# Optimization experiments

Measured on AMD Instinct MI355X. Metric: run time of the kernel, lower is better.

The kernel has to match this reference:

```python
import jax, jax.numpy as jnp
import numpy as np

D = 1024        # node_dim
L = 4           # n_layers
H = 16          # n_heads
HID = 512       # mlp_hidden
NT = 65536      # N_tiles (256x256 board)
U = 4096        # eligible units
NY = 256        # board width


def setup_inputs() -> dict:
    key = jax.random.key(0)
    ks = jax.random.split(key, 32)
    p = lambda i, shape: jax.random.normal(ks[i], shape, jnp.float32) * 0.02
    inp = {
        "node_emb": jax.random.normal(ks[0], (NT, D), jnp.float32),
        "tile_ids": jax.random.randint(ks[1], (U,), 0, NT),
        "entropies": jax.random.uniform(ks[2], (U,), jnp.float32),
        "Ny": NY,
        # input_proj: Linear(D+1, D), torch weight layout (out, in)
        "in_w": p(3, (D, D + 1)), "in_b": p(4, (D,)),
        # per-layer MHA params stacked over L
        "attn_in_w": p(5, (L, 3 * D, D)), "attn_in_b": p(6, (L, 3 * D)),
        "attn_out_w": p(7, (L, D, D)), "attn_out_b": p(8, (L, D)),
        # per-layer FFN: Linear(D, 2D) -> ReLU -> Linear(2D, D)
        "ff_w1": p(9, (L, 2 * D, D)), "ff_b1": p(10, (L, 2 * D)),
        "ff_w2": p(11, (L, D, 2 * D)), "ff_b2": p(12, (L, D)),
        "ln1_g": jnp.ones((L, D), jnp.float32), "ln1_b": jnp.zeros((L, D), jnp.float32),
        "ln2_g": jnp.ones((L, D), jnp.float32), "ln2_b": jnp.zeros((L, D), jnp.float32),
        # score head: D -> HID -> HID -> 1 (mlp_depth=2)
        "sh_w0": p(13, (HID, D)), "sh_b0": p(14, (HID,)),
        "sh_w1": p(15, (HID, HID)), "sh_b1": p(16, (HID,)),
        "sh_w2": p(17, (1, HID)), "sh_b2": p(18, (1,)),
    }
    return inp


def _rope_1d(x, pos):
    half = x.shape[-1] // 2
    theta = 1.0 / (10000.0 ** (jnp.arange(half, dtype=jnp.float32) / half))
    ang = pos[:, None] * theta[None, :]            # (U, half)
    c, s = jnp.cos(ang), jnp.sin(ang)
    x1, x2 = x[..., :half], x[..., half:]
    return jnp.concatenate([x1 * c - x2 * s, x1 * s + x2 * c], axis=-1)


def _ln(x, g, b, eps=1e-5):
    m = x.mean(-1, keepdims=True)
    v = ((x - m) ** 2).mean(-1, keepdims=True)
    return (x - m) / jnp.sqrt(v + eps) * g + b


def reference(node_emb, tile_ids, entropies, Ny, in_w, in_b,
              attn_in_w, attn_in_b, attn_out_w, attn_out_b,
              ff_w1, ff_b1, ff_w2, ff_b2, ln1_g, ln1_b, ln2_g, ln2_b,
              sh_w0, sh_b0, sh_w1, sh_b1, sh_w2, sh_b2):
    u = node_emb[tile_ids]                                   # (U, D)
    x = jnp.concatenate([u, entropies[:, None]], axis=-1) @ in_w.T + in_b
    n_units, d = x.shape
    half = d // 2
    hd = d // H
    rows = (tile_ids // Ny).astype(jnp.float32)
    cols = (tile_ids % Ny).astype(jnp.float32)
    for l in range(L):
        # 2D RoPE: row rotation on first half of dims, col rotation on second
        xr = jnp.concatenate([_rope_1d(x[:, :half], rows),
                              _rope_1d(x[:, half:], cols)], axis=-1)
        wq, wk, wv = jnp.split(attn_in_w[l], 3, axis=0)
        bq, bk, bv = jnp.split(attn_in_b[l], 3, axis=0)
        q = (xr @ wq.T + bq).reshape(n_units, H, hd)
        k = (xr @ wk.T + bk).reshape(n_units, H, hd)
        v = (x @ wv.T + bv).reshape(n_units, H, hd)          # V from un-roped x
        scores = jnp.einsum("qhd,khd->hqk", q, k) / jnp.sqrt(jnp.float32(hd))
        attn = jax.nn.softmax(scores, axis=-1)
        o = jnp.einsum("hqk,khd->qhd", attn, v).reshape(n_units, d)
        o = o @ attn_out_w[l].T + attn_out_b[l]
        x = _ln(x + o, ln1_g[l], ln1_b[l])
        h = jax.nn.relu(x @ ff_w1[l].T + ff_b1[l]) @ ff_w2[l].T + ff_b2[l]
        x = _ln(x + h, ln2_g[l], ln2_b[l])
    h = jax.nn.relu(x @ sh_w0.T + sh_b0)
    h = jax.nn.relu(h @ sh_w1.T + sh_b1)
    logits = (h @ sh_w2.T + sh_b2).squeeze(-1)               # (U,)
    probs = jax.nn.softmax(logits)
    entropy = -(probs * jnp.log(probs + 1e-12)).sum()
    return (probs, entropy, logits)
```

## Files before the change

kernel.cpp:

```cpp
#include <hip/hip_runtime.h>
#include <hip/hip_bf16.h>
#include <math.h>

#define UN 4096
#define DN 1024
#define LN_ 4
#define HN 16
#define HD 64

typedef __attribute__((ext_vector_type(8))) short bf16x8;
typedef __attribute__((ext_vector_type(4))) float f32x4;

__device__ __forceinline__ short f2bf(float f) {
  union { float f; unsigned u; } x; x.f = f;
  unsigned r = x.u + 0x7fffu + ((x.u >> 16) & 1u);
  return (short)(r >> 16);
}
__device__ __forceinline__ float bf2f(short b) {
  union { unsigned u; float f; } x; x.u = ((unsigned)(unsigned short)b) << 16;
  return x.f;
}

__device__ __forceinline__ void gload16(const void* g, void* l) {
  __builtin_amdgcn_global_load_lds(
      (const __attribute__((address_space(1))) void*)g,
      (__attribute__((address_space(3))) void*)l, 16, 0, 0);
}

__global__ __launch_bounds__(256)
void convw_kernel(const float* __restrict__ src, short* __restrict__ dst)
{
  int i = blockIdx.x * 256 + threadIdx.x;
  float4 f0 = ((const float4*)src)[i * 2];
  float4 f1 = ((const float4*)src)[i * 2 + 1];
  bf16x8 o;
  o[0] = f2bf(f0.x); o[1] = f2bf(f0.y); o[2] = f2bf(f0.z); o[3] = f2bf(f0.w);
  o[4] = f2bf(f1.x); o[5] = f2bf(f1.y); o[6] = f2bf(f1.z); o[7] = f2bf(f1.w);
  ((bf16x8*)dst)[i] = o;
}

__global__ __launch_bounds__(256)
void convw_in_kernel(const float* __restrict__ src, short* __restrict__ dst)
{
  int idx = blockIdx.x * 256 + threadIdx.x;
  int r = idx >> 10, c = idx & 1023;
  dst[idx] = f2bf(src[r * 1025 + c]);
}

template<int TM>
__global__ __launch_bounds__(256)
void gemm_bf16(const short* __restrict__ A, int lda,
               const short* __restrict__ W, int ldw,
               const float* __restrict__ bias,
               float* __restrict__ C32, short* __restrict__ C16, int ldc,
               int K, int relu,
               const float* __restrict__ ent, const float* __restrict__ wcol,
               int wstride)
{
  constexpr int MBF = TM / 32;
  constexpr int AIN = TM / 64;
  __shared__ __align__(16) short As[TM][32];
  __shared__ __align__(16) short Ws[128][32];

  const int tid  = threadIdx.x;
  const int bm = blockIdx.x, bn = blockIdx.y;
  const int lane = tid & 63, wave = tid >> 6;
  const int n = lane & 15, quad = lane >> 4;
  const int mw = (wave >> 1) * (TM / 2), nw = (wave & 1) * 64;

  f32x4 acc[MBF][4];
#pragma unroll
  for (int mb = 0; mb < MBF; mb++)
#pragma unroll
    for (int nb = 0; nb < 4; nb++)
#pragma unroll
      for (int r = 0; r < 4; r++) acc[mb][nb][r] = 0.f;

  const int sr = lane >> 2;
  const int sc = (lane & 3) * 8;
  const short* aSrc[AIN]; short* aDst[AIN];
#pragma unroll
  for (int i = 0; i < AIN; i++) {
    aSrc[i] = A + (size_t)(bm * TM + wave * (16 * AIN) + i * 16 + sr) * lda + sc;
    aDst[i] = &As[wave * (16 * AIN) + i * 16][0];
  }
  const short* wSrc[2]; short* wDst[2];
#pragma unroll
  for (int i = 0; i < 2; i++) {
    wSrc[i] = W + (size_t)(bn * 128 + wave * 32 + i * 16 + sr) * ldw + sc;
    wDst[i] = &Ws[wave * 32 + i * 16][0];
  }

  for (int kk = 0; kk < K; kk += 32) {
    __syncthreads();
#pragma unroll
    for (int i = 0; i < AIN; i++) gload16(aSrc[i] + kk, aDst[i]);
#pragma unroll
    for (int i = 0; i < 2; i++)   gload16(wSrc[i] + kk, wDst[i]);
    __syncthreads();

    bf16x8 af[MBF], bfr[4];
#pragma unroll
    for (int mb = 0; mb < MBF; mb++) af[mb] = *(bf16x8*)&As[mw + mb * 16 + n][quad * 8];
#pragma unroll
    for (int nb = 0; nb < 4; nb++)   bfr[nb] = *(bf16x8*)&Ws[nw + nb * 16 + n][quad * 8];
#pragma unroll
    for (int mb = 0; mb < MBF; mb++)
#pragma unroll
      for (int nb = 0; nb < 4; nb++)
        acc[mb][nb] = __builtin_amdgcn_mfma_f32_16x16x32_bf16(af[mb], bfr[nb], acc[mb][nb], 0, 0, 0);
  }

#pragma unroll
  for (int mb = 0; mb < MBF; mb++) {
    float entv[4];
#pragma unroll
    for (int r = 0; r < 4; r++)
      entv[r] = ent ? ent[bm * TM + mw + mb * 16 + quad * 4 + r] : 0.f;
#pragma unroll
    for (int nb = 0; nb < 4; nb++) {
      const int col = bn * 128 + nw + nb * 16 + n;
      const float bs = bias[col];
      const float wc = ent ? wcol[(size_t)col * wstride] : 0.f;
#pragma unroll
      for (int r = 0; r < 4; r++) {
        const int row = bm * TM + mw + mb * 16 + quad * 4 + r;
        float v = acc[mb][nb][r] + bs;
        if (ent)  v += entv[r] * wc;
        if (relu) v = fmaxf(v, 0.f);
        if (C32) C32[(size_t)row * ldc + col] = v;
        if (C16) C16[(size_t)row * ldc + col] = f2bf(v);
      }
    }
  }
}

__global__ __launch_bounds__(256)
void gather_conv_kernel(const float* __restrict__ emb, const int* __restrict__ ids,
                        short* __restrict__ dst)
{
  int idx = blockIdx.x * 256 + threadIdx.x;
  int u = idx >> 10;
  dst[idx] = f2bf(emb[(size_t)ids[u] * 1024 + (idx & 1023)]);
}

__global__ __launch_bounds__(256)
void rope_kernel(const float* __restrict__ x, short* __restrict__ xr,
                 const int* __restrict__ ids, const int* __restrict__ nyp)
{
  int idx = blockIdx.x * 256 + threadIdx.x;
  int u = idx >> 10, j = idx & 1023;
  int blk = j >> 9, o = j & 511;
  int i = o & 255;
  int t = ids[u];
  int ny = *nyp;
  float pos = (blk == 0) ? (float)(t / ny) : (float)(t % ny);
  float theta = expf((float)i * -0.0359778921f);
  float ang = pos * theta;
  float c = cosf(ang), sn = sinf(ang);
  const float* xrow = x + (size_t)u * 1024 + blk * 512;
  float x1 = xrow[i];
  float x2 = xrow[256 + i];
  xr[idx] = f2bf((o < 256) ? (x1 * c - x2 * sn) : (x1 * sn + x2 * c));
}

__global__ __launch_bounds__(256)
void attn_mfma_kernel(const short* __restrict__ qk, const short* __restrict__ v,
                      short* __restrict__ o)
{
  __shared__ __align__(16) short Kt[64][64];
  __shared__ __align__(16) short Vt[64][64];
  __shared__ __align__(16) short Pb[4][16][64];

  const int tid  = threadIdx.x;
  const int lane = tid & 63;
  const int wave = tid >> 6;
  const int head = blockIdx.y;
  const int qb   = blockIdx.x;

  const int n    = lane & 15;
  const int quad = lane >> 4;

  bf16x8 qfrag[2];
  {
    const int qrow = qb * 64 + wave * 16 + n;
    const short* qptr = qk + (size_t)qrow * 2048 + head * 64 + quad * 8;
#pragma unroll
    for (int c = 0; c < 2; c++)
#pragma unroll
      for (int j = 0; j < 8; j++)
        qfrag[c][j] = f2bf(bf2f(qptr[c * 32 + j]) * 0.125f);
  }

  float m_r[4], l_r[4];
  f32x4 o_acc[4];
#pragma unroll
  for (int r = 0; r < 4; r++) { m_r[r] = -3.0e38f; l_r[r] = 0.f; }
#pragma unroll
  for (int nb = 0; nb < 4; nb++)
#pragma unroll
    for (int r = 0; r < 4; r++) o_acc[nb][r] = 0.f;

  const int skey = tid & 63;
  const int sd0  = wave * 16;
  const int krx  = (skey & 7) << 4;

  char* KtB = (char*)&Kt[0][0];
  char* VtB = (char*)&Vt[0][0];
  char* PbB = (char*)&Pb[wave][0][0];

  for (int kt = 0; kt < 64; kt++) {
    __syncthreads();
    {
      const short* kp = qk + (size_t)(kt * 64 + skey) * 2048 + 1024 + head * 64 + sd0;
      bf16x8 k0 = *(const bf16x8*)(kp);
      bf16x8 k1 = *(const bf16x8*)(kp + 8);
      *(bf16x8*)(KtB + skey * 128 + ((sd0 * 2)      ^ krx)) = k0;
      *(bf16x8*)(KtB + skey * 128 + ((sd0 * 2 + 16) ^ krx)) = k1;
      const short* vp = v + (size_t)(kt * 64 + skey) * 1024 + head * 64 + sd0;
      bf16x8 v0 = *(const bf16x8*)(vp);
      bf16x8 v1 = *(const bf16x8*)(vp + 8);
#pragma unroll
      for (int i = 0; i < 8; i++) {
        int d = sd0 + i;
        *(short*)(VtB + d * 128 + ((2 * skey) ^ ((d & 7) << 4))) = v0[i];
      }
#pragma unroll
      for (int i = 0; i < 8; i++) {
        int d = sd0 + 8 + i;
        *(short*)(VtB + d * 128 + ((2 * skey) ^ ((d & 7) << 4))) = v1[i];
      }
    }
    __syncthreads();

    f32x4 s[4];
#pragma unroll
    for (int nb = 0; nb < 4; nb++) {
      const int row = nb * 16 + n;
      const int rx = (row & 7) << 4;
      bf16x8 k0 = *(bf16x8*)(KtB + row * 128 + ((quad * 16)      ^ rx));
      bf16x8 k1 = *(bf16x8*)(KtB + row * 128 + ((64 + quad * 16) ^ rx));
      f32x4 z = {0.f, 0.f, 0.f, 0.f};
      z = __builtin_amdgcn_mfma_f32_16x16x32_bf16(qfrag[0], k0, z, 0, 0, 0);
      z = __builtin_amdgcn_mfma_f32_16x16x32_bf16(qfrag[1], k1, z, 0, 0, 0);
      s[nb] = z;
    }

    float tl[4];
#pragma unroll
    for (int r = 0; r < 4; r++)
      tl[r] = fmaxf(fmaxf(s[0][r], s[1][r]), fmaxf(s[2][r], s[3][r]));
    bool grow = (tl[0] > m_r[0] + 8.f) || (tl[1] > m_r[1] + 8.f) ||
                (tl[2] > m_r[2] + 8.f) || (tl[3] > m_r[3] + 8.f);
    if (__any(grow)) {
#pragma unroll
      for (int r = 0; r < 4; r++) {
        float t = tl[r];
        t = fmaxf(t, __shfl_xor(t, 1));
        t = fmaxf(t, __shfl_xor(t, 2));
        t = fmaxf(t, __shfl_xor(t, 4));
        t = fmaxf(t, __shfl_xor(t, 8));
        float mnew = fmaxf(m_r[r], t);
        float al = __expf(m_r[r] - mnew);
        m_r[r] = mnew;
        l_r[r] *= al;
#pragma unroll
        for (int nb = 0; nb < 4; nb++) o_acc[nb][r] *= al;
      }
    }

    float rs[4] = {0.f, 0.f, 0.f, 0.f};
#pragma unroll
    for (int nb = 0; nb < 4; nb++) {
      float p0 = __expf(s[nb][0] - m_r[0]);
      float p1 = __expf(s[nb][1] - m_r[1]);
      float p2 = __expf(s[nb][2] - m_r[2]);
      float p3 = __expf(s[nb][3] - m_r[3]);
      rs[0] += p0; rs[1] += p1; rs[2] += p2; rs[3] += p3;
      unsigned u01, u23;
      asm("v_cvt_pk_bf16_f32 %0, %1, %2" : "=v"(u01) : "v"(p0), "v"(p1));
      asm("v_cvt_pk_bf16_f32 %0, %1, %2" : "=v"(u23) : "v"(p2), "v"(p3));
      const int colb = 2 * (nb * 16 + n);
      const int r0 = quad * 4;
      *(short*)(PbB + (r0 + 0) * 128 + (colb ^ (((r0 + 0) & 7) << 4))) = (short)(u01 & 0xffff);
      *(short*)(PbB + (r0 + 1) * 128 + (colb ^ (((r0 + 1) & 7) << 4))) = (short)(u01 >> 16);
      *(short*)(PbB + (r0 + 2) * 128 + (colb ^ (((r0 + 2) & 7) << 4))) = (short)(u23 & 0xffff);
      *(short*)(PbB + (r0 + 3) * 128 + (colb ^ (((r0 + 3) & 7) << 4))) = (short)(u23 >> 16);
    }
#pragma unroll
    for (int r = 0; r < 4; r++) {
      float t = rs[r];
      t += __shfl_xor(t, 1); t += __shfl_xor(t, 2);
      t += __shfl_xor(t, 4); t += __shfl_xor(t, 8);
      l_r[r] += t;
    }

#pragma unroll
    for (int c = 0; c < 2; c++) {
      const int prx = (n & 7) << 4;
      bf16x8 pf = *(bf16x8*)(PbB + n * 128 + ((64 * c + 16 * quad) ^ prx));
#pragma unroll
      for (int nb = 0; nb < 4; nb++) {
        const int row = nb * 16 + n;
        const int rx = (row & 7) << 4;
        bf16x8 vf = *(bf16x8*)(VtB + row * 128 + ((64 * c + 16 * quad) ^ rx));
        o_acc[nb] = __builtin_amdgcn_mfma_f32_16x16x32_bf16(pf, vf, o_acc[nb], 0, 0, 0);
      }
    }
  }

#pragma unroll
  for (int r = 0; r < 4; r++) l_r[r] = 1.f / l_r[r];
#pragma unroll
  for (int nb = 0; nb < 4; nb++)
#pragma unroll
    for (int r = 0; r < 4; r++) {
      int row = qb * 64 + wave * 16 + quad * 4 + r;
      o[(size_t)row * 1024 + head * 64 + nb * 16 + n] = f2bf(o_acc[nb][r] * l_r[r]);
    }
}

__global__ __launch_bounds__(256)
void add_ln_kernel(float* __restrict__ x, const float* __restrict__ d,
                   const float* __restrict__ g, const float* __restrict__ b,
                   short* __restrict__ xb)
{
  __shared__ float sb[4];
  const int row = blockIdx.x, tid = threadIdx.x;
  float* xr = x + (size_t)row * 1024;
  const float* dr = d + (size_t)row * 1024;

  float v[4]; float s = 0.f, ss = 0.f;
#pragma unroll
  for (int i = 0; i < 4; i++) {
    int c = tid + 256 * i;
    v[i] = xr[c] + dr[c];
    s += v[i]; ss += v[i] * v[i];
  }
#pragma unroll
  for (int off = 32; off; off >>= 1) { s += __shfl_down(s, off); ss += __shfl_down(ss, off); }
  const int lane = tid & 63, wid = tid >> 6;
  if (lane == 0) sb[wid] = s;
  __syncthreads();
  s = sb[0] + sb[1] + sb[2] + sb[3];
  __syncthreads();
  if (lane == 0) sb[wid] = ss;
  __syncthreads();
  ss = sb[0] + sb[1] + sb[2] + sb[3];

  float mean = s * (1.f / 1024.f);
  float var  = ss * (1.f / 1024.f) - mean * mean;
  float inv  = rsqrtf(var + 1e-5f);
#pragma unroll
  for (int i = 0; i < 4; i++) {
    int c = tid + 256 * i;
    float o = (v[i] - mean) * inv * g[c] + b[c];
    xr[c] = o;
    xb[(size_t)row * 1024 + c] = f2bf(o);
  }
}

__global__ __launch_bounds__(256)
void logits_kernel(const float* __restrict__ h1, const float* __restrict__ w2,
                   const float* __restrict__ b2, float* __restrict__ out)
{
  const int lane = threadIdx.x & 63;
  const int row = blockIdx.x * 4 + (threadIdx.x >> 6);
  const float* hr = h1 + (size_t)row * 512;
  float s = 0.f;
#pragma unroll
  for (int i = 0; i < 8; i++) s += hr[lane + 64 * i] * w2[lane + 64 * i];
#pragma unroll
  for (int off = 32; off; off >>= 1) s += __shfl_down(s, off);
  if (lane == 0) {
    out[4097 + row] = s + b2[0];
  }
}

__global__ __launch_bounds__(1024)
void softmax_entropy_kernel(const float* __restrict__ lg, float* __restrict__ out)
{
  __shared__ float sb[16];
  const int tid = threadIdx.x;
  const int lane = tid & 63, wid = tid >> 6;

  float l0[4];
#pragma unroll
  for (int i = 0; i < 4; i++) l0[i] = lg[tid + 1024 * i];

  float mx = fmaxf(fmaxf(l0[0], l0[1]), fmaxf(l0[2], l0[3]));
#pragma unroll
  for (int off = 32; off; off >>= 1) mx = fmaxf(mx, __shfl_down(mx, off));
  if (lane == 0) sb[wid] = mx;
  __syncthreads();
  if (tid == 0) { float m = sb[0]; for (int i = 1; i < 16; i++) m = fmaxf(m, sb[i]); sb[0] = m; }
  __syncthreads();
  mx = sb[0];
  __syncthreads();

  float e[4], s = 0.f;
#pragma unroll
  for (int i = 0; i < 4; i++) { e[i] = expf(l0[i] - mx); s += e[i]; }
#pragma unroll
  for (int off = 32; off; off >>= 1) s += __shfl_down(s, off);
  if (lane == 0) sb[wid] = s;
  __syncthreads();
  if (tid == 0) { float t = 0.f; for (int i = 0; i < 16; i++) t += sb[i]; sb[0] = t; }
  __syncthreads();
  float inv = 1.f / sb[0];
  __syncthreads();

  float h = 0.f;
#pragma unroll
  for (int i = 0; i < 4; i++) {
    float p = e[i] * inv;
    out[tid + 1024 * i] = p;
    h += p * logf(p + 1e-12f);
  }
#pragma unroll
  for (int off = 32; off; off >>= 1) h += __shfl_down(h, off);
  if (lane == 0) sb[wid] = h;
  __syncthreads();
  if (tid == 0) { float t = 0.f; for (int i = 0; i < 16; i++) t += sb[i]; out[4096] = -t; }
}

extern "C" void kernel_launch(void* const* d_in, const int* in_sizes, int n_in,
                              void* d_out, int out_size, void* d_ws, size_t ws_size,
                              hipStream_t stream)
{
  const float* node_emb   = (const float*)d_in[0];
  const int*   tile_ids   = (const int*)d_in[1];
  const float* entropies  = (const float*)d_in[2];
  const int*   Ny_p       = (const int*)d_in[3];
  const float* in_w       = (const float*)d_in[4];
  const float* in_b       = (const float*)d_in[5];
  const float* attn_in_w  = (const float*)d_in[6];
  const float* attn_in_b  = (const float*)d_in[7];
  const float* attn_out_w = (const float*)d_in[8];
  const float* attn_out_b = (const float*)d_in[9];
  const float* ff_w1      = (const float*)d_in[10];
  const float* ff_b1      = (const float*)d_in[11];
  const float* ff_w2      = (const float*)d_in[12];
  const float* ff_b2      = (const float*)d_in[13];
  const float* ln1_g      = (const float*)d_in[14];
  const float* ln1_b      = (const float*)d_in[15];
  const float* ln2_g      = (const float*)d_in[16];
  const float* ln2_b      = (const float*)d_in[17];
  const float* sh_w0      = (const float*)d_in[18];
  const float* sh_b0      = (const float*)d_in[19];
  const float* sh_w1      = (const float*)d_in[20];
  const float* sh_b1      = (const float*)d_in[21];
  const float* sh_w2      = (const float*)d_in[22];
  const float* sh_b2      = (const float*)d_in[23];
  float* out = (float*)d_out;

  char* w8 = (char*)d_ws;
  float* X    = (float*)(w8);
  short* Xb   = (short*)(w8 + (16u << 20));
  short* XRb  = (short*)(w8 + (24u << 20));
  short* QKb  = (short*)(w8 + (32u << 20));
  short* Vb   = (short*)(w8 + (48u << 20));
  short* Ob   = (short*)(w8 + (56u << 20));
  float* O2   = (float*)(w8 + (64u << 20));
  short* Wb   = (short*)(w8 + (80u << 20));
  short* Hb   = QKb;
  short* A0b  = Ob;
  short* H0b  = XRb;
  float* H1   = (float*)(w8 + (32u << 20));

  gather_conv_kernel<<<UN * DN / 256, 256, 0, stream>>>(node_emb, tile_ids, A0b);

  convw_in_kernel<<<DN * DN / 256, 256, 0, stream>>>(in_w, Wb);
  gemm_bf16<64><<<dim3(64, 8), 256, 0, stream>>>(A0b, 1024, Wb, 1024, in_b,
      X, Xb, 1024, 1024, 0, entropies, in_w + 1024, 1025);

  for (int l = 0; l < LN_; l++) {
    const float* b_qkv = attn_in_b + (size_t)l * 3 * DN;

    convw_kernel<<<3 * DN * DN / 2048, 256, 0, stream>>>(attn_in_w + (size_t)l * 3 * DN * DN, Wb);
    rope_kernel<<<UN * DN / 256, 256, 0, stream>>>(X, XRb, tile_ids, Ny_p);
    gemm_bf16<128><<<dim3(32, 16), 256, 0, stream>>>(XRb, 1024, Wb, 1024, b_qkv,
        nullptr, QKb, 2048, 1024, 0, nullptr, nullptr, 0);
    gemm_bf16<64><<<dim3(64, 8), 256, 0, stream>>>(Xb, 1024, Wb + (size_t)2048 * 1024, 1024,
        b_qkv + 2048, nullptr, Vb, 1024, 1024, 0, nullptr, nullptr, 0);
    attn_mfma_kernel<<<dim3(UN / 64, HN), 256, 0, stream>>>(QKb, Vb, Ob);
    convw_kernel<<<DN * DN / 2048, 256, 0, stream>>>(attn_out_w + (size_t)l * DN * DN, Wb);
    gemm_bf16<64><<<dim3(64, 8), 256, 0, stream>>>(Ob, 1024, Wb, 1024,
        attn_out_b + (size_t)l * DN, O2, nullptr, 1024, 1024, 0, nullptr, nullptr, 0);
    add_ln_kernel<<<UN, 256, 0, stream>>>(X, O2, ln1_g + (size_t)l * DN, ln1_b + (size_t)l * DN, Xb);
    convw_kernel<<<2 * DN * DN / 2048, 256, 0, stream>>>(ff_w1 + (size_t)l * 2 * DN * DN, Wb);
    gemm_bf16<128><<<dim3(32, 16), 256, 0, stream>>>(Xb, 1024, Wb, 1024,
        ff_b1 + (size_t)l * 2 * DN, nullptr, Hb, 2048, 1024, 1, nullptr, nullptr, 0);
    convw_kernel<<<2 * DN * DN / 2048, 256, 0, stream>>>(ff_w2 + (size_t)l * DN * 2 * DN, Wb);
    gemm_bf16<64><<<dim3(64, 8), 256, 0, stream>>>(Hb, 2048, Wb, 2048,
        ff_b2 + (size_t)l * DN, O2, nullptr, 1024, 2048, 0, nullptr, nullptr, 0);
    add_ln_kernel<<<UN, 256, 0, stream>>>(X, O2, ln2_g + (size_t)l * DN, ln2_b + (size_t)l * DN, Xb);
  }

  convw_kernel<<<512 * DN / 2048, 256, 0, stream>>>(sh_w0, Wb);
  gemm_bf16<64><<<dim3(64, 4), 256, 0, stream>>>(Xb, 1024, Wb, 1024, sh_b0,
      nullptr, H0b, 512, 1024, 1, nullptr, nullptr, 0);
  convw_kernel<<<512 * 512 / 2048, 256, 0, stream>>>(sh_w1, Wb);
  gemm_bf16<64><<<dim3(64, 4), 256, 0, stream>>>(H0b, 512, Wb, 512, sh_b1,
      H1, nullptr, 512, 512, 1, nullptr, nullptr, 0);
  logits_kernel<<<UN / 4, 256, 0, stream>>>(H1, sh_w2, sh_b2, out);
  softmax_entropy_kernel<<<1, 1024, 0, stream>>>(out + 4097, out);
}
```

Baseline: 2.049 ms.

## Double-buffer GEMM LDS tiles and software-pipeline attention K/V loads

The GEMM now double-buffers its A/W shared-memory tiles, issuing the next tile's global-to-LDS loads before computing on the current one and using explicit vmcnt waits plus raw barriers instead of two __syncthreads per step. The attention kernel prefetches the next K/V tile into registers while computing the current one, remaps workgroup IDs across heads, and raises MFMA priority with s_setprio. It also defers the row-sum shuffle reduction of the softmax denominator to the end and changes the LDS swizzle index on reads to (n&7). The aim is to hide global memory latency and cut sync and shuffle overhead, at the cost of twice the GEMM LDS and more registers in attention.

```diff
diff --git a/kernel.cpp b/kernel.cpp
--- a/kernel.cpp
+++ b/kernel.cpp
@@ -10,6 +10,10 @@
 
 typedef __attribute__((ext_vector_type(8))) short bf16x8;
 typedef __attribute__((ext_vector_type(4))) float f32x4;
+
+#define LGKM0 asm volatile("s_waitcnt lgkmcnt(0)" ::: "memory")
+#define BARRIER0 __builtin_amdgcn_s_barrier()
+#define SCHED0 __builtin_amdgcn_sched_barrier(0)
 
 __device__ __forceinline__ short f2bf(float f) {
   union { float f; unsigned u; } x; x.f = f;
@@ -59,8 +63,9 @@
 {
   constexpr int MBF = TM / 32;
   constexpr int AIN = TM / 64;
-  __shared__ __align__(16) short As[TM][32];
-  __shared__ __align__(16) short Ws[128][32];
+  constexpr int NLD = AIN + 2;
+  __shared__ __align__(16) short As[2][TM][32];
+  __shared__ __align__(16) short Ws[2][128][32];
 
   const int tid  = threadIdx.x;
   const int bm = blockIdx.x, bn = blockIdx.y;
@@ -78,37 +83,48 @@
 
   const int sr = lane >> 2;
   const int sc = (lane & 3) * 8;
-  const short* aSrc[AIN]; short* aDst[AIN];
-#pragma unroll
-  for (int i = 0; i < AIN; i++) {
+  const short* aSrc[AIN];
+#pragma unroll
+  for (int i = 0; i < AIN; i++)
     aSrc[i] = A + (size_t)(bm * TM + wave * (16 * AIN) + i * 16 + sr) * lda + sc;
-    aDst[i] = &As[wave * (16 * AIN) + i * 16][0];
-  }
-  const short* wSrc[2]; short* wDst[2];
-#pragma unroll
-  for (int i = 0; i < 2; i++) {
+  const short* wSrc[2];
+#pragma unroll
+  for (int i = 0; i < 2; i++)
     wSrc[i] = W + (size_t)(bn * 128 + wave * 32 + i * 16 + sr) * ldw + sc;
-    wDst[i] = &Ws[wave * 32 + i * 16][0];
-  }
-
+
+  auto stage = [&](int buf, int kk) {
+#pragma unroll
+    for (int i = 0; i < AIN; i++)
+      gload16(aSrc[i] + kk, &As[buf][wave * (16 * AIN) + i * 16][0]);
+#pragma unroll
+    for (int i = 0; i < 2; i++)
+      gload16(wSrc[i] + kk, &Ws[buf][wave * 32 + i * 16][0]);
+  };
+
+  stage(0, 0);
+  int cur = 0;
   for (int kk = 0; kk < K; kk += 32) {
-    __syncthreads();
-#pragma unroll
-    for (int i = 0; i < AIN; i++) gload16(aSrc[i] + kk, aDst[i]);
-#pragma unroll
-    for (int i = 0; i < 2; i++)   gload16(wSrc[i] + kk, wDst[i]);
-    __syncthreads();
+    if (kk + 32 < K) {
+      stage(cur ^ 1, kk + 32);
+      asm volatile("s_waitcnt vmcnt(%0)" :: "n"(NLD) : "memory");
+    } else {
+      asm volatile("s_waitcnt vmcnt(0)" ::: "memory");
+    }
+    BARRIER0; SCHED0;
 
     bf16x8 af[MBF], bfr[4];
 #pragma unroll
-    for (int mb = 0; mb < MBF; mb++) af[mb] = *(bf16x8*)&As[mw + mb * 16 + n][quad * 8];
-#pragma unroll
-    for (int nb = 0; nb < 4; nb++)   bfr[nb] = *(bf16x8*)&Ws[nw + nb * 16 + n][quad * 8];
+    for (int mb = 0; mb < MBF; mb++) af[mb] = *(bf16x8*)&As[cur][mw + mb * 16 + n][quad * 8];
+#pragma unroll
+    for (int nb = 0; nb < 4; nb++)   bfr[nb] = *(bf16x8*)&Ws[cur][nw + nb * 16 + n][quad * 8];
 #pragma unroll
     for (int mb = 0; mb < MBF; mb++)
 #pragma unroll
       for (int nb = 0; nb < 4; nb++)
         acc[mb][nb] = __builtin_amdgcn_mfma_f32_16x16x32_bf16(af[mb], bfr[nb], acc[mb][nb], 0, 0, 0);
+
+    LGKM0; BARRIER0; SCHED0;
+    cur ^= 1;
   }
 
 #pragma unroll
@@ -175,8 +191,11 @@
   const int tid  = threadIdx.x;
   const int lane = tid & 63;
   const int wave = tid >> 6;
-  const int head = blockIdx.y;
-  const int qb   = blockIdx.x;
+
+  int wg = blockIdx.x + 64 * blockIdx.y;
+  wg = (wg & 7) * 128 + (wg >> 3);
+  const int qb   = wg & 63;
+  const int head = wg >> 6;
 
   const int n    = lane & 15;
   const int quad = lane >> 4;
@@ -209,40 +228,43 @@
   char* VtB = (char*)&Vt[0][0];
   char* PbB = (char*)&Pb[wave][0][0];
 
-  for (int kt = 0; kt < 64; kt++) {
-    __syncthreads();
-    {
-      const short* kp = qk + (size_t)(kt * 64 + skey) * 2048 + 1024 + head * 64 + sd0;
-      bf16x8 k0 = *(const bf16x8*)(kp);
-      bf16x8 k1 = *(const bf16x8*)(kp + 8);
-      *(bf16x8*)(KtB + skey * 128 + ((sd0 * 2)      ^ krx)) = k0;
-      *(bf16x8*)(KtB + skey * 128 + ((sd0 * 2 + 16) ^ krx)) = k1;
-      const short* vp = v + (size_t)(kt * 64 + skey) * 1024 + head * 64 + sd0;
-      bf16x8 v0 = *(const bf16x8*)(vp);
-      bf16x8 v1 = *(const bf16x8*)(vp + 8);
-#pragma unroll
-      for (int i = 0; i < 8; i++) {
-        int d = sd0 + i;
-        *(short*)(VtB + d * 128 + ((2 * skey) ^ ((d & 7) << 4))) = v0[i];
-      }
-#pragma unroll
-      for (int i = 0; i < 8; i++) {
-        int d = sd0 + 8 + i;
-        *(short*)(VtB + d * 128 + ((2 * skey) ^ ((d & 7) << 4))) = v1[i];
-      }
-    }
-    __syncthreads();
-
+  auto loadT = [&](int kt, bf16x8& k0, bf16x8& k1, bf16x8& v0, bf16x8& v1) {
+    const short* kp = qk + (size_t)(kt * 64 + skey) * 2048 + 1024 + head * 64 + sd0;
+    k0 = *(const bf16x8*)(kp);
+    k1 = *(const bf16x8*)(kp + 8);
+    const short* vp = v + (size_t)(kt * 64 + skey) * 1024 + head * 64 + sd0;
+    v0 = *(const bf16x8*)(vp);
+    v1 = *(const bf16x8*)(vp + 8);
+  };
+
+  auto writeT = [&](bf16x8 k0, bf16x8 k1, bf16x8 v0, bf16x8 v1) {
+    *(bf16x8*)(KtB + skey * 128 + ((sd0 * 2)      ^ krx)) = k0;
+    *(bf16x8*)(KtB + skey * 128 + ((sd0 * 2 + 16) ^ krx)) = k1;
+#pragma unroll
+    for (int i = 0; i < 8; i++) {
+      int d = sd0 + i;
+      *(short*)(VtB + d * 128 + ((2 * skey) ^ ((d & 7) << 4))) = v0[i];
+    }
+#pragma unroll
+    for (int i = 0; i < 8; i++) {
+      int d = sd0 + 8 + i;
+      *(short*)(VtB + d * 128 + ((2 * skey) ^ ((d & 7) << 4))) = v1[i];
+    }
+  };
+
+  auto computeT = [&]() {
     f32x4 s[4];
 #pragma unroll
     for (int nb = 0; nb < 4; nb++) {
       const int row = nb * 16 + n;
-      const int rx = (row & 7) << 4;
+      const int rx = (n & 7) << 4;
       bf16x8 k0 = *(bf16x8*)(KtB + row * 128 + ((quad * 16)      ^ rx));
       bf16x8 k1 = *(bf16x8*)(KtB + row * 128 + ((64 + quad * 16) ^ rx));
       f32x4 z = {0.f, 0.f, 0.f, 0.f};
+      __builtin_amdgcn_s_setprio(1);
       z = __builtin_amdgcn_mfma_f32_16x16x32_bf16(qfrag[0], k0, z, 0, 0, 0);
       z = __builtin_amdgcn_mfma_f32_16x16x32_bf16(qfrag[1], k1, z, 0, 0, 0);
+      __builtin_amdgcn_s_setprio(0);
       s[nb] = z;
     }
 
@@ -269,14 +291,13 @@
       }
     }
 
-    float rs[4] = {0.f, 0.f, 0.f, 0.f};
 #pragma unroll
     for (int nb = 0; nb < 4; nb++) {
       float p0 = __expf(s[nb][0] - m_r[0]);
       float p1 = __expf(s[nb][1] - m_r[1]);
       float p2 = __expf(s[nb][2] - m_r[2]);
       float p3 = __expf(s[nb][3] - m_r[3]);
-      rs[0] += p0; rs[1] += p1; rs[2] += p2; rs[3] += p3;
+      l_r[0] += p0; l_r[1] += p1; l_r[2] += p2; l_r[3] += p3;
       unsigned u01, u23;
       asm("v_cvt_pk_bf16_f32 %0, %1, %2" : "=v"(u01) : "v"(p0), "v"(p1));
       asm("v_cvt_pk_bf16_f32 %0, %1, %2" : "=v"(u23) : "v"(p2), "v"(p3));
@@ -287,13 +308,6 @@
       *(short*)(PbB + (r0 + 2) * 128 + (colb ^ (((r0 + 2) & 7) << 4))) = (short)(u23 & 0xffff);
       *(short*)(PbB + (r0 + 3) * 128 + (colb ^ (((r0 + 3) & 7) << 4))) = (short)(u23 >> 16);
     }
-#pragma unroll
-    for (int r = 0; r < 4; r++) {
-      float t = rs[r];
-      t += __shfl_xor(t, 1); t += __shfl_xor(t, 2);
-      t += __shfl_xor(t, 4); t += __shfl_xor(t, 8);
-      l_r[r] += t;
-    }
 
 #pragma unroll
     for (int c = 0; c < 2; c++) {
@@ -302,15 +316,38 @@
 #pragma unroll
       for (int nb = 0; nb < 4; nb++) {
         const int row = nb * 16 + n;
-        const int rx = (row & 7) << 4;
+        const int rx = (n & 7) << 4;
         bf16x8 vf = *(bf16x8*)(VtB + row * 128 + ((64 * c + 16 * quad) ^ rx));
+        __builtin_amdgcn_s_setprio(1);
         o_acc[nb] = __builtin_amdgcn_mfma_f32_16x16x32_bf16(pf, vf, o_acc[nb], 0, 0, 0);
+        __builtin_amdgcn_s_setprio(0);
       }
     }
-  }
-
-#pragma unroll
-  for (int r = 0; r < 4; r++) l_r[r] = 1.f / l_r[r];
+  };
+
+  bf16x8 ka0, ka1, va0, va1, kb0, kb1, vb0, vb1;
+  loadT(0, ka0, ka1, va0, va1);
+  for (int kt = 0; kt < 64; kt += 2) {
+    LGKM0; BARRIER0; SCHED0;
+    writeT(ka0, ka1, va0, va1);
+    loadT(kt + 1, kb0, kb1, vb0, vb1);
+    LGKM0; BARRIER0; SCHED0;
+    computeT();
+
+    LGKM0; BARRIER0; SCHED0;
+    writeT(kb0, kb1, vb0, vb1);
+    if (kt + 2 < 64) loadT(kt + 2, ka0, ka1, va0, va1);
+    LGKM0; BARRIER0; SCHED0;
+    computeT();
+  }
+
+#pragma unroll
+  for (int r = 0; r < 4; r++) {
+    float t = l_r[r];
+    t += __shfl_xor(t, 1); t += __shfl_xor(t, 2);
+    t += __shfl_xor(t, 4); t += __shfl_xor(t, 8);
+    l_r[r] = 1.f / t;
+  }
 #pragma unroll
   for (int nb = 0; nb < 4; nb++)
 #pragma unroll
```

Result: faster. 1.968 ms (-3.9%).
